# Kernel tuning notes

Hardware: AMD Instinct MI355X
Metric: run time of the kernel (lower is better)

The kernel has to match this reference:

```python
import jax, jax.numpy as jnp
import numpy as np
import math

N = 8192
IN_FEATURES = 512
OUT_FEATURES = 64
NEG_INF = -9e15

def setup_inputs() -> dict:
    key = jax.random.key(0)
    k1, k2, k3, k4 = jax.random.split(key, 4)
    inp = jax.random.normal(k1, (N, IN_FEATURES), dtype=jnp.float32)
    adj = jax.random.randint(k2, (N, N), 0, 2, dtype=jnp.int32)
    # xavier_uniform with gain=1.414 for [in, out] weights
    limit = 1.414 * math.sqrt(6.0 / (IN_FEATURES + OUT_FEATURES))
    kW = jax.random.uniform(k3, (IN_FEATURES, OUT_FEATURES), dtype=jnp.float32, minval=-limit, maxval=limit)
    vW = jax.random.uniform(k4, (IN_FEATURES, OUT_FEATURES), dtype=jnp.float32, minval=-limit, maxval=limit)
    return {"input": inp, "adj": adj, "kW": kW, "vW": vW}

def reference(input, adj, kW, vW):
    kh = input @ kW                      # [N, d]
    vh = input @ vW                      # [N, d]
    d = kh.shape[1]
    K = (kh @ kh.T) / jnp.sqrt(jnp.asarray(d, dtype=kh.dtype))  # [N, N]
    scores = jnp.where(adj > 0, K, jnp.asarray(NEG_INF, dtype=K.dtype))
    attention = jax.nn.softmax(scores, axis=1)
    # dropout is a no-op (p=0.0 / eval mode)
    h_prime = attention @ vh             # [N, d]
    return jax.nn.elu(h_prime)           # concat=True path
```

## Files before the change

kernel.cpp:

```cpp
#include <hip/hip_runtime.h>
#include <math.h>

typedef __bf16 bf16_t;
typedef __bf16 bf16x8 __attribute__((ext_vector_type(8)));
typedef float f32x4 __attribute__((ext_vector_type(4)));

#define NN 8192
#define L2E 1.44269504088896340736f
#define SMAX 45.0f
#define KSCALE 0.35355339059327373f

__global__ __launch_bounds__(256) void conv_kernel(
    const float* __restrict__ input,
    const float* __restrict__ kW,
    const float* __restrict__ vW,
    bf16_t* __restrict__ inputH,
    bf16_t* __restrict__ inputL,
    bf16_t* __restrict__ wimgH,
    bf16_t* __restrict__ wimgL)
{
    const int b = blockIdx.x;
    if (b < 2048) {
        const size_t idx = ((size_t)b * 256 + threadIdx.x) * 8;
        f32x4 a0 = *(const f32x4*)&input[idx];
        f32x4 a1 = *(const f32x4*)&input[idx + 4];
        bf16x8 h8, l8;
        #pragma unroll
        for (int j = 0; j < 4; ++j) {
            bf16_t h0 = (bf16_t)a0[j], h1 = (bf16_t)a1[j];
            h8[j]     = h0;  l8[j]     = (bf16_t)(a0[j] - (float)h0);
            h8[4 + j] = h1;  l8[4 + j] = (bf16_t)(a1[j] - (float)h1);
        }
        *(bf16x8*)&inputH[idx] = h8;
        *(bf16x8*)&inputL[idx] = l8;
    } else {
        const int gid  = (b - 2048) * 256 + threadIdx.x;
        const int proj = gid >> 12;
        const int r    = gid & 4095;
        const int frag = r >> 6;
        const int lane = r & 63;
        const int kc   = frag >> 2;
        const int nb   = frag & 3;
        const int quad = lane >> 4;
        const int l15  = lane & 15;
        const float* W = proj ? vW : kW;
        bf16x8 h8, l8;
        #pragma unroll
        for (int j = 0; j < 8; ++j) {
            float w  = W[(size_t)(kc * 32 + quad * 8 + j) * 64 + nb * 16 + l15];
            bf16_t h = (bf16_t)w;
            h8[j] = h;
            l8[j] = (bf16_t)(w - (float)h);
        }
        ((bf16x8*)wimgH)[gid] = h8;
        ((bf16x8*)wimgL)[gid] = l8;
    }
}

__global__ __launch_bounds__(256) void pack_adj(
    const int* __restrict__ adj, unsigned int* __restrict__ bits)
{
    const int lane = threadIdx.x & 63;
    const int gw   = blockIdx.x * 4 + (threadIdx.x >> 6);
    const int nw   = gridDim.x * 4;
    const int nchunks = (NN / 256) * NN;
    for (int c = gw; c < nchunks; c += nw) {
        const int* p = adj + (size_t)c * 256;
        unsigned int* o = bits + (size_t)c * 8;
        #pragma unroll
        for (int k = 0; k < 4; ++k) {
            int v = p[k * 64 + lane];
            unsigned long long m = __ballot(v > 0);
            if (lane == 0) *(uint2*)(o + 2 * k) = *(uint2*)&m;
        }
    }
}

__global__ __launch_bounds__(512) void proj_kernel(
    const bf16_t* __restrict__ inputH,
    const bf16_t* __restrict__ inputL,
    const bf16_t* __restrict__ wimgH,
    const bf16_t* __restrict__ wimgL,
    bf16_t* __restrict__ khs_hi,
    bf16_t* __restrict__ khs_lo,
    bf16_t* __restrict__ vhT)
{
    const int tid   = threadIdx.x;
    const int w     = tid >> 6;
    const int lane  = tid & 63;
    const int proj  = w >> 2;
    const int nb    = w & 3;
    const int l15   = lane & 15;
    const int quad  = lane >> 4;
    const int rbase = blockIdx.x * 16;

    const bf16x8* ah_p = (const bf16x8*)&inputH[(size_t)(rbase + l15) * 512 + quad * 8];
    const bf16x8* al_p = (const bf16x8*)&inputL[(size_t)(rbase + l15) * 512 + quad * 8];
    const bf16x8* bh_p = (const bf16x8*)wimgH + ((size_t)proj * 64 + nb) * 64 + lane;
    const bf16x8* bl_p = (const bf16x8*)wimgL + ((size_t)proj * 64 + nb) * 64 + lane;

    f32x4 acc = {};
    #pragma unroll
    for (int kc = 0; kc < 16; ++kc) {
        bf16x8 ah = ah_p[kc * 4];
        bf16x8 al = al_p[kc * 4];
        bf16x8 bh = bh_p[(size_t)kc * 256];
        bf16x8 bl = bl_p[(size_t)kc * 256];
        acc = __builtin_amdgcn_mfma_f32_16x16x32_bf16(ah, bh, acc, 0, 0, 0);
        acc = __builtin_amdgcn_mfma_f32_16x16x32_bf16(al, bh, acc, 0, 0, 0);
        acc = __builtin_amdgcn_mfma_f32_16x16x32_bf16(ah, bl, acc, 0, 0, 0);
    }

    const int dcol = nb * 16 + l15;
    if (proj == 0) {
        #pragma unroll
        for (int r = 0; r < 4; ++r) {
            float v  = acc[r] * KSCALE;
            bf16_t h = (bf16_t)v;
            khs_hi[(size_t)(rbase + quad * 4 + r) * 64 + dcol] = h;
            khs_lo[(size_t)(rbase + quad * 4 + r) * 64 + dcol] = (bf16_t)(v - (float)h);
        }
    } else {
        union { bf16_t b[4]; uint2 u; } pk;
        #pragma unroll
        for (int r = 0; r < 4; ++r) pk.b[r] = (bf16_t)acc[r];
        *(uint2*)&vhT[(size_t)dcol * NN + rbase + quad * 4] = pk.u;
    }
}

__global__ __launch_bounds__(512, 4) void attn_kernel(
    const unsigned int* __restrict__ bits,
    const bf16_t* __restrict__ khs_hi,
    const bf16_t* __restrict__ khs_lo,
    const bf16_t* __restrict__ vhT,
    float* __restrict__ out)
{
    __shared__ __align__(16) float PlBuf[8 * 1152];

    const int tid   = threadIdx.x;
    const int w     = tid >> 6;
    const int lane  = tid & 63;
    const int l15   = lane & 15;
    const int quad  = lane >> 4;
    const int qbase = blockIdx.x * 16;
    const int colstart = w * 1024;

    const bf16x8 qh0 = *(const bf16x8*)&khs_hi[(size_t)(qbase + l15) * 64 + quad * 8];
    const bf16x8 qh1 = *(const bf16x8*)&khs_hi[(size_t)(qbase + l15) * 64 + 32 + quad * 8];
    const bf16x8 ql0 = *(const bf16x8*)&khs_lo[(size_t)(qbase + l15) * 64 + quad * 8];
    const bf16x8 ql1 = *(const bf16x8*)&khs_lo[(size_t)(qbase + l15) * 64 + 32 + quad * 8];

    bf16x8 ones;
    #pragma unroll
    for (int j = 0; j < 8; ++j) ones[j] = (bf16_t)1.0f;

    f32x4 o0 = {}, o1 = {}, o2 = {}, o3 = {}, o4 = {};

    const unsigned int* bp = bits + (size_t)(qbase + quad * 4) * 256 + (colstart >> 5);

    unsigned int wcur[4], wnxt[4];
    #pragma unroll
    for (int r = 0; r < 4; ++r) wcur[r] = bp[r * 256];

    for (int t = 0; t < 32; ++t) {
        const int colbase = colstart + t * 32;
        float* Plw = &PlBuf[w * 1152 + (t & 1) * 576];

        const bf16_t* kph = khs_hi + (size_t)(colbase + l15) * 64 + quad * 8;
        bf16x8 bh00 = *(const bf16x8*)(kph);
        bf16x8 bh01 = *(const bf16x8*)(kph + 32);
        bf16x8 bh10 = *(const bf16x8*)(kph + 16 * 64);
        bf16x8 bh11 = *(const bf16x8*)(kph + 16 * 64 + 32);
        const bf16_t* vp = vhT + (size_t)l15 * NN + colbase + quad * 8;
        bf16x8 bv0 = *(const bf16x8*)(vp);
        bf16x8 bv1 = *(const bf16x8*)(vp + (size_t)16 * NN);
        bf16x8 bv2 = *(const bf16x8*)(vp + (size_t)32 * NN);
        bf16x8 bv3 = *(const bf16x8*)(vp + (size_t)48 * NN);

        const int tn = (t + 1) & 31;
        #pragma unroll
        for (int r = 0; r < 4; ++r) wnxt[r] = bp[r * 256 + tn];

        f32x4 zz = {};
        f32x4 s0 = __builtin_amdgcn_mfma_f32_16x16x32_bf16(qh0, bh00, zz, 0, 0, 0);
        s0 = __builtin_amdgcn_mfma_f32_16x16x32_bf16(qh1, bh01, s0, 0, 0, 0);
        s0 = __builtin_amdgcn_mfma_f32_16x16x32_bf16(ql0, bh00, s0, 0, 0, 0);
        s0 = __builtin_amdgcn_mfma_f32_16x16x32_bf16(ql1, bh01, s0, 0, 0, 0);
        f32x4 s1 = __builtin_amdgcn_mfma_f32_16x16x32_bf16(qh0, bh10, zz, 0, 0, 0);
        s1 = __builtin_amdgcn_mfma_f32_16x16x32_bf16(qh1, bh11, s1, 0, 0, 0);
        s1 = __builtin_amdgcn_mfma_f32_16x16x32_bf16(ql0, bh10, s1, 0, 0, 0);
        s1 = __builtin_amdgcn_mfma_f32_16x16x32_bf16(ql1, bh11, s1, 0, 0, 0);

        #pragma unroll
        for (int r = 0; r < 4; ++r) {
            float p0 = ((wcur[r] >> l15) & 1u)        ? __builtin_amdgcn_exp2f((s0[r] - SMAX) * L2E) : 0.f;
            float p1 = ((wcur[r] >> (16 + l15)) & 1u) ? __builtin_amdgcn_exp2f((s1[r] - SMAX) * L2E) : 0.f;
            Plw[(quad * 4 + r) * 36 + l15]      = p0;
            Plw[(quad * 4 + r) * 36 + 16 + l15] = p1;
        }

        __asm__ __volatile__("s_waitcnt lgkmcnt(0)" ::: "memory");

        f32x4 pfa = *(const f32x4*)&Plw[l15 * 36 + quad * 8];
        f32x4 pfb = *(const f32x4*)&Plw[l15 * 36 + quad * 8 + 4];
        bf16x8 pa;
        #pragma unroll
        for (int j = 0; j < 4; ++j) { pa[j] = (bf16_t)pfa[j]; pa[4 + j] = (bf16_t)pfb[j]; }

        o0 = __builtin_amdgcn_mfma_f32_16x16x32_bf16(pa, bv0, o0, 0, 0, 0);
        o1 = __builtin_amdgcn_mfma_f32_16x16x32_bf16(pa, bv1, o1, 0, 0, 0);
        o2 = __builtin_amdgcn_mfma_f32_16x16x32_bf16(pa, bv2, o2, 0, 0, 0);
        o3 = __builtin_amdgcn_mfma_f32_16x16x32_bf16(pa, bv3, o3, 0, 0, 0);
        o4 = __builtin_amdgcn_mfma_f32_16x16x32_bf16(pa, ones, o4, 0, 0, 0);

        #pragma unroll
        for (int r = 0; r < 4; ++r) wcur[r] = wnxt[r];
    }

    float* M = PlBuf;
    #pragma unroll
    for (int s = 4; s >= 1; s >>= 1) {
        __syncthreads();
        if (w >= s && w < 2 * s) {
            float* base = M + (w - s) * 16 * 68;
            #pragma unroll
            for (int r = 0; r < 4; ++r) {
                const int row = quad * 4 + r;
                base[row * 68 + l15]      = o0[r];
                base[row * 68 + 16 + l15] = o1[r];
                base[row * 68 + 32 + l15] = o2[r];
                base[row * 68 + 48 + l15] = o3[r];
                if (l15 == 0) base[row * 68 + 64] = o4[r];
            }
        }
        __syncthreads();
        if (w < s) {
            float* base = M + w * 16 * 68;
            #pragma unroll
            for (int r = 0; r < 4; ++r) {
                const int row = quad * 4 + r;
                o0[r] += base[row * 68 + l15];
                o1[r] += base[row * 68 + 16 + l15];
                o2[r] += base[row * 68 + 32 + l15];
                o3[r] += base[row * 68 + 48 + l15];
                o4[r] += base[row * 68 + 64];
            }
        }
    }

    if (w == 0) {
        #pragma unroll
        for (int r = 0; r < 4; ++r) {
            const size_t row = (size_t)qbase + quad * 4 + r;
            float l   = o4[r];
            float inv = 1.0f / (l > 0.f ? l : 1.0f);
            float v0 = o0[r] * inv, v1 = o1[r] * inv, v2 = o2[r] * inv, v3 = o3[r] * inv;
            out[row * 64 + l15]      = v0 > 0.f ? v0 : expm1f(v0);
            out[row * 64 + 16 + l15] = v1 > 0.f ? v1 : expm1f(v1);
            out[row * 64 + 32 + l15] = v2 > 0.f ? v2 : expm1f(v2);
            out[row * 64 + 48 + l15] = v3 > 0.f ? v3 : expm1f(v3);
        }
    }
}

extern "C" void kernel_launch(void* const* d_in, const int* in_sizes, int n_in,
                              void* d_out, int out_size, void* d_ws, size_t ws_size,
                              hipStream_t stream) {
    const float* input = nullptr;
    const int*   adj   = nullptr;
    const float* kW    = nullptr;
    const float* vW    = nullptr;
    for (int i = 0; i < n_in; ++i) {
        if (in_sizes[i] == 8192 * 512)            input = (const float*)d_in[i];
        else if (in_sizes[i] == 512 * 64) {
            if (!kW) kW = (const float*)d_in[i]; else vW = (const float*)d_in[i];
        } else                                    adj = (const int*)d_in[i];
    }
    float* out = (float*)d_out;

    char* ws = (char*)d_ws;
    bf16_t*       khs_hi = (bf16_t*)(ws);
    bf16_t*       khs_lo = (bf16_t*)(ws + (1u << 20));
    bf16_t*       vhT    = (bf16_t*)(ws + (2u << 20));
    unsigned int* bits   = (unsigned int*)(ws + (3u << 20));
    bf16_t*       inputH = (bf16_t*)(ws + (11u << 20));
    bf16_t*       inputL = (bf16_t*)(ws + (19u << 20));
    bf16_t*       wimgH  = (bf16_t*)(ws + (27u << 20));
    bf16_t*       wimgL  = (bf16_t*)(ws + (27u << 20) + (128u << 10));

    conv_kernel<<<2080, 256, 0, stream>>>(input, kW, vW, inputH, inputL, wimgH, wimgL);
    pack_adj<<<2048, 256, 0, stream>>>(adj, bits);
    proj_kernel<<<512, 512, 0, stream>>>(inputH, inputL, wimgH, wimgL, khs_hi, khs_lo, vhT);
    attn_kernel<<<512, 512, 0, stream>>>(bits, khs_hi, khs_lo, vhT, out);
}
```

Before: 529.7 us.

## Split attention columns across two blocks with atomic accumulation and fuse prep kernels

The attention kernel now gives each 16-row block two column halves handled by separate blocks, doubling the grid and halving the loop length. Partial numerators and denominators are combined with atomicAdd into a zeroed workspace, and a new finalize kernel applies normalization and ELU. The input/weight conversion, adjacency bit-packing and accumulator zeroing are merged into one launch to cut launch overhead. The aim is better CU utilization for the attention stage, at the cost of atomic traffic, an extra finalize kernel and a tighter occupancy hint.

```diff
diff --git a/kernel.cpp b/kernel.cpp
--- a/kernel.cpp
+++ b/kernel.cpp
@@ -9,15 +9,19 @@
 #define L2E 1.44269504088896340736f
 #define SMAX 45.0f
 #define KSCALE 0.35355339059327373f
-
-__global__ __launch_bounds__(256) void conv_kernel(
+#define ACCW 66
+
+__global__ __launch_bounds__(256) void prep_kernel(
     const float* __restrict__ input,
     const float* __restrict__ kW,
     const float* __restrict__ vW,
+    const int*   __restrict__ adj,
     bf16_t* __restrict__ inputH,
     bf16_t* __restrict__ inputL,
     bf16_t* __restrict__ wimgH,
-    bf16_t* __restrict__ wimgL)
+    bf16_t* __restrict__ wimgL,
+    unsigned int* __restrict__ bits,
+    float* __restrict__ acc)
 {
     const int b = blockIdx.x;
     if (b < 2048) {
@@ -33,7 +37,7 @@
         }
         *(bf16x8*)&inputH[idx] = h8;
         *(bf16x8*)&inputL[idx] = l8;
-    } else {
+    } else if (b < 2080) {
         const int gid  = (b - 2048) * 256 + threadIdx.x;
         const int proj = gid >> 12;
         const int r    = gid & 4095;
@@ -54,25 +58,25 @@
         }
         ((bf16x8*)wimgH)[gid] = h8;
         ((bf16x8*)wimgL)[gid] = l8;
-    }
-}
-
-__global__ __launch_bounds__(256) void pack_adj(
-    const int* __restrict__ adj, unsigned int* __restrict__ bits)
-{
-    const int lane = threadIdx.x & 63;
-    const int gw   = blockIdx.x * 4 + (threadIdx.x >> 6);
-    const int nw   = gridDim.x * 4;
-    const int nchunks = (NN / 256) * NN;
-    for (int c = gw; c < nchunks; c += nw) {
-        const int* p = adj + (size_t)c * 256;
-        unsigned int* o = bits + (size_t)c * 8;
-        #pragma unroll
-        for (int k = 0; k < 4; ++k) {
-            int v = p[k * 64 + lane];
-            unsigned long long m = __ballot(v > 0);
-            if (lane == 0) *(uint2*)(o + 2 * k) = *(uint2*)&m;
-        }
+    } else if (b < 4128) {
+        const int lane = threadIdx.x & 63;
+        const int gw   = (b - 2080) * 4 + (threadIdx.x >> 6);
+        const int nw   = 2048 * 4;
+        const int nchunks = (NN / 256) * NN;
+        for (int c = gw; c < nchunks; c += nw) {
+            const int* p = adj + (size_t)c * 256;
+            unsigned int* o = bits + (size_t)c * 8;
+            #pragma unroll
+            for (int k = 0; k < 4; ++k) {
+                int v = p[k * 64 + lane];
+                unsigned long long m = __ballot(v > 0);
+                if (lane == 0) *(uint2*)(o + 2 * k) = *(uint2*)&m;
+            }
+        }
+    } else {
+        const size_t idx = ((size_t)(b - 4128) * 256 + threadIdx.x) * 4;
+        f32x4 z = {};
+        *(f32x4*)&acc[idx] = z;
     }
 }
 
@@ -128,12 +132,12 @@
     }
 }
 
-__global__ __launch_bounds__(512, 4) void attn_kernel(
+__global__ __launch_bounds__(512, 8) void attn_kernel(
     const unsigned int* __restrict__ bits,
     const bf16_t* __restrict__ khs_hi,
     const bf16_t* __restrict__ khs_lo,
     const bf16_t* __restrict__ vhT,
-    float* __restrict__ out)
+    float* __restrict__ acc)
 {
     __shared__ __align__(16) float PlBuf[8 * 1152];
 
@@ -142,8 +146,10 @@
     const int lane  = tid & 63;
     const int l15   = lane & 15;
     const int quad  = lane >> 4;
-    const int qbase = blockIdx.x * 16;
-    const int colstart = w * 1024;
+    const int rb    = blockIdx.x >> 1;
+    const int ch    = blockIdx.x & 1;
+    const int qbase = rb * 16;
+    const int colstart = ch * 4096 + w * 512;
 
     const bf16x8 qh0 = *(const bf16x8*)&khs_hi[(size_t)(qbase + l15) * 64 + quad * 8];
     const bf16x8 qh1 = *(const bf16x8*)&khs_hi[(size_t)(qbase + l15) * 64 + 32 + quad * 8];
@@ -162,7 +168,7 @@
     #pragma unroll
     for (int r = 0; r < 4; ++r) wcur[r] = bp[r * 256];
 
-    for (int t = 0; t < 32; ++t) {
+    for (int t = 0; t < 16; ++t) {
         const int colbase = colstart + t * 32;
         float* Plw = &PlBuf[w * 1152 + (t & 1) * 576];
 
@@ -177,7 +183,7 @@
         bf16x8 bv2 = *(const bf16x8*)(vp + (size_t)32 * NN);
         bf16x8 bv3 = *(const bf16x8*)(vp + (size_t)48 * NN);
 
-        const int tn = (t + 1) & 31;
+        const int tn = (t + 1) & 15;
         #pragma unroll
         for (int r = 0; r < 4; ++r) wnxt[r] = bp[r * 256 + tn];
 
@@ -252,15 +258,21 @@
         #pragma unroll
         for (int r = 0; r < 4; ++r) {
             const size_t row = (size_t)qbase + quad * 4 + r;
-            float l   = o4[r];
-            float inv = 1.0f / (l > 0.f ? l : 1.0f);
-            float v0 = o0[r] * inv, v1 = o1[r] * inv, v2 = o2[r] * inv, v3 = o3[r] * inv;
-            out[row * 64 + l15]      = v0 > 0.f ? v0 : expm1f(v0);
-            out[row * 64 + 16 + l15] = v1 > 0.f ? v1 : expm1f(v1);
-            out[row * 64 + 32 + l15] = v2 > 0.f ? v2 : expm1f(v2);
-            out[row * 64 + 48 + l15] = v3 > 0.f ? v3 : expm1f(v3);
-        }
-    }
+            atomicAdd(&acc[row * ACCW + l15],      o0[r]);
+            atomicAdd(&acc[row * ACCW + 16 + l15], o1[r]);
+            atomicAdd(&acc[row * ACCW + 32 + l15], o2[r]);
+            atomicAdd(&acc[row * ACCW + 48 + l15], o3[r]);
+            if (l15 == 0) atomicAdd(&acc[row * ACCW + 64], o4[r]);
+        }
+    }
+}
+
+__global__ void finalize(const float* __restrict__ acc, float* __restrict__ out) {
+    int i = blockIdx.x * blockDim.x + threadIdx.x;
+    int row = i >> 6, d = i & 63;
+    float l = acc[(size_t)row * ACCW + 64];
+    float v = acc[(size_t)row * ACCW + d] / (l > 0.f ? l : 1.f);
+    out[i] = v > 0.f ? v : expm1f(v);
 }
 
 extern "C" void kernel_launch(void* const* d_in, const int* in_sizes, int n_in,
@@ -287,9 +299,11 @@
     bf16_t*       inputL = (bf16_t*)(ws + (19u << 20));
     bf16_t*       wimgH  = (bf16_t*)(ws + (27u << 20));
     bf16_t*       wimgL  = (bf16_t*)(ws + (27u << 20) + (128u << 10));
-
-    conv_kernel<<<2080, 256, 0, stream>>>(input, kW, vW, inputH, inputL, wimgH, wimgL);
-    pack_adj<<<2048, 256, 0, stream>>>(adj, bits);
+    float*        acc    = (float*)(ws + (28u << 20));
+
+    prep_kernel<<<4656, 256, 0, stream>>>(input, kW, vW, adj,
+                                          inputH, inputL, wimgH, wimgL, bits, acc);
     proj_kernel<<<512, 512, 0, stream>>>(inputH, inputL, wimgH, wimgL, khs_hi, khs_lo, vhT);
-    attn_kernel<<<512, 512, 0, stream>>>(bits, khs_hi, khs_lo, vhT, out);
-}
+    attn_kernel<<<1024, 512, 0, stream>>>(bits, khs_hi, khs_lo, vhT, acc);
+    finalize<<<(NN * 64) / 512, 512, 0, stream>>>(acc, out);
+}
```

Result: slower. 623.7 us (+17.7%).

## Fuse adjacency packing into prep kernel and swap LDS P round-trip for bpermute

Applied to the files above, without the earlier changes.

The adjacency bit-packing kernel is merged into the input/weight conversion kernel as extra blocks, which removes one launch and lets the two independent prep jobs run concurrently. In the attention kernel the score MFMA operands are swapped so each lane holds a transposed score tile. The probabilities are packed to bf16 in registers and redistributed with ds_bpermute instead of being written to LDS as floats and read back. This cuts LDS traffic and the explicit waitcnt, and shrinks shared memory, which may allow more occupancy. The cost is eight bpermutes per step and some select logic.

```diff
diff --git a/kernel.cpp b/kernel.cpp
--- a/kernel.cpp
+++ b/kernel.cpp
@@ -10,14 +10,16 @@
 #define SMAX 45.0f
 #define KSCALE 0.35355339059327373f
 
-__global__ __launch_bounds__(256) void conv_kernel(
+__global__ __launch_bounds__(256) void prep_kernel(
     const float* __restrict__ input,
     const float* __restrict__ kW,
     const float* __restrict__ vW,
+    const int*   __restrict__ adj,
     bf16_t* __restrict__ inputH,
     bf16_t* __restrict__ inputL,
     bf16_t* __restrict__ wimgH,
-    bf16_t* __restrict__ wimgL)
+    bf16_t* __restrict__ wimgL,
+    unsigned int* __restrict__ bits)
 {
     const int b = blockIdx.x;
     if (b < 2048) {
@@ -33,7 +35,7 @@
         }
         *(bf16x8*)&inputH[idx] = h8;
         *(bf16x8*)&inputL[idx] = l8;
-    } else {
+    } else if (b < 2080) {
         const int gid  = (b - 2048) * 256 + threadIdx.x;
         const int proj = gid >> 12;
         const int r    = gid & 4095;
@@ -54,24 +56,20 @@
         }
         ((bf16x8*)wimgH)[gid] = h8;
         ((bf16x8*)wimgL)[gid] = l8;
-    }
-}
-
-__global__ __launch_bounds__(256) void pack_adj(
-    const int* __restrict__ adj, unsigned int* __restrict__ bits)
-{
-    const int lane = threadIdx.x & 63;
-    const int gw   = blockIdx.x * 4 + (threadIdx.x >> 6);
-    const int nw   = gridDim.x * 4;
-    const int nchunks = (NN / 256) * NN;
-    for (int c = gw; c < nchunks; c += nw) {
-        const int* p = adj + (size_t)c * 256;
-        unsigned int* o = bits + (size_t)c * 8;
-        #pragma unroll
-        for (int k = 0; k < 4; ++k) {
-            int v = p[k * 64 + lane];
-            unsigned long long m = __ballot(v > 0);
-            if (lane == 0) *(uint2*)(o + 2 * k) = *(uint2*)&m;
+    } else {
+        const int lane = threadIdx.x & 63;
+        const int gw   = (b - 2080) * 4 + (threadIdx.x >> 6);
+        const int nw   = 2048 * 4;
+        const int nchunks = (NN / 256) * NN;
+        for (int c = gw; c < nchunks; c += nw) {
+            const int* p = adj + (size_t)c * 256;
+            unsigned int* o = bits + (size_t)c * 8;
+            #pragma unroll
+            for (int k = 0; k < 4; ++k) {
+                int v = p[k * 64 + lane];
+                unsigned long long m = __ballot(v > 0);
+                if (lane == 0) *(uint2*)(o + 2 * k) = *(uint2*)&m;
+            }
         }
     }
 }
@@ -135,7 +133,7 @@
     const bf16_t* __restrict__ vhT,
     float* __restrict__ out)
 {
-    __shared__ __align__(16) float PlBuf[8 * 1152];
+    __shared__ __align__(16) float M[4 * 16 * 68];
 
     const int tid   = threadIdx.x;
     const int w     = tid >> 6;
@@ -156,15 +154,14 @@
 
     f32x4 o0 = {}, o1 = {}, o2 = {}, o3 = {}, o4 = {};
 
-    const unsigned int* bp = bits + (size_t)(qbase + quad * 4) * 256 + (colstart >> 5);
-
-    unsigned int wcur[4], wnxt[4];
-    #pragma unroll
-    for (int r = 0; r < 4; ++r) wcur[r] = bp[r * 256];
+    const unsigned int* bpl = bits + (size_t)(qbase + l15) * 256 + (colstart >> 5);
+    unsigned int mcur = bpl[0], mnxt;
+
+    const int idxA = (l15 + (((2 * quad)    ) & 3) * 16) * 4;
+    const int idxB = (l15 + (((2 * quad) | 1) & 3) * 16) * 4;
 
     for (int t = 0; t < 32; ++t) {
         const int colbase = colstart + t * 32;
-        float* Plw = &PlBuf[w * 1152 + (t & 1) * 576];
 
         const bf16_t* kph = khs_hi + (size_t)(colbase + l15) * 64 + quad * 8;
         bf16x8 bh00 = *(const bf16x8*)(kph);
@@ -177,47 +174,53 @@
         bf16x8 bv2 = *(const bf16x8*)(vp + (size_t)32 * NN);
         bf16x8 bv3 = *(const bf16x8*)(vp + (size_t)48 * NN);
 
-        const int tn = (t + 1) & 31;
-        #pragma unroll
-        for (int r = 0; r < 4; ++r) wnxt[r] = bp[r * 256 + tn];
+        mnxt = bpl[(t + 1) & 31];
 
         f32x4 zz = {};
-        f32x4 s0 = __builtin_amdgcn_mfma_f32_16x16x32_bf16(qh0, bh00, zz, 0, 0, 0);
-        s0 = __builtin_amdgcn_mfma_f32_16x16x32_bf16(qh1, bh01, s0, 0, 0, 0);
-        s0 = __builtin_amdgcn_mfma_f32_16x16x32_bf16(ql0, bh00, s0, 0, 0, 0);
-        s0 = __builtin_amdgcn_mfma_f32_16x16x32_bf16(ql1, bh01, s0, 0, 0, 0);
-        f32x4 s1 = __builtin_amdgcn_mfma_f32_16x16x32_bf16(qh0, bh10, zz, 0, 0, 0);
-        s1 = __builtin_amdgcn_mfma_f32_16x16x32_bf16(qh1, bh11, s1, 0, 0, 0);
-        s1 = __builtin_amdgcn_mfma_f32_16x16x32_bf16(ql0, bh10, s1, 0, 0, 0);
-        s1 = __builtin_amdgcn_mfma_f32_16x16x32_bf16(ql1, bh11, s1, 0, 0, 0);
-
+        f32x4 s0 = __builtin_amdgcn_mfma_f32_16x16x32_bf16(bh00, qh0, zz, 0, 0, 0);
+        s0 = __builtin_amdgcn_mfma_f32_16x16x32_bf16(bh01, qh1, s0, 0, 0, 0);
+        s0 = __builtin_amdgcn_mfma_f32_16x16x32_bf16(bh00, ql0, s0, 0, 0, 0);
+        s0 = __builtin_amdgcn_mfma_f32_16x16x32_bf16(bh01, ql1, s0, 0, 0, 0);
+        f32x4 s1 = __builtin_amdgcn_mfma_f32_16x16x32_bf16(bh10, qh0, zz, 0, 0, 0);
+        s1 = __builtin_amdgcn_mfma_f32_16x16x32_bf16(bh11, qh1, s1, 0, 0, 0);
+        s1 = __builtin_amdgcn_mfma_f32_16x16x32_bf16(bh10, ql0, s1, 0, 0, 0);
+        s1 = __builtin_amdgcn_mfma_f32_16x16x32_bf16(bh11, ql1, s1, 0, 0, 0);
+
+        union { bf16_t b[2]; int u; } k0, k1, k2, k3;
         #pragma unroll
         for (int r = 0; r < 4; ++r) {
-            float p0 = ((wcur[r] >> l15) & 1u)        ? __builtin_amdgcn_exp2f((s0[r] - SMAX) * L2E) : 0.f;
-            float p1 = ((wcur[r] >> (16 + l15)) & 1u) ? __builtin_amdgcn_exp2f((s1[r] - SMAX) * L2E) : 0.f;
-            Plw[(quad * 4 + r) * 36 + l15]      = p0;
-            Plw[(quad * 4 + r) * 36 + 16 + l15] = p1;
-        }
-
-        __asm__ __volatile__("s_waitcnt lgkmcnt(0)" ::: "memory");
-
-        f32x4 pfa = *(const f32x4*)&Plw[l15 * 36 + quad * 8];
-        f32x4 pfb = *(const f32x4*)&Plw[l15 * 36 + quad * 8 + 4];
-        bf16x8 pa;
-        #pragma unroll
-        for (int j = 0; j < 4; ++j) { pa[j] = (bf16_t)pfa[j]; pa[4 + j] = (bf16_t)pfb[j]; }
-
-        o0 = __builtin_amdgcn_mfma_f32_16x16x32_bf16(pa, bv0, o0, 0, 0, 0);
-        o1 = __builtin_amdgcn_mfma_f32_16x16x32_bf16(pa, bv1, o1, 0, 0, 0);
-        o2 = __builtin_amdgcn_mfma_f32_16x16x32_bf16(pa, bv2, o2, 0, 0, 0);
-        o3 = __builtin_amdgcn_mfma_f32_16x16x32_bf16(pa, bv3, o3, 0, 0, 0);
-        o4 = __builtin_amdgcn_mfma_f32_16x16x32_bf16(pa, ones, o4, 0, 0, 0);
-
-        #pragma unroll
-        for (int r = 0; r < 4; ++r) wcur[r] = wnxt[r];
-    }
-
-    float* M = PlBuf;
+            float p0 = ((mcur >> (quad * 4 + r)) & 1u)
+                         ? __builtin_amdgcn_exp2f((s0[r] - SMAX) * L2E) : 0.f;
+            float p1 = ((mcur >> (16 + quad * 4 + r)) & 1u)
+                         ? __builtin_amdgcn_exp2f((s1[r] - SMAX) * L2E) : 0.f;
+            if (r < 2) { k0.b[r] = (bf16_t)p0; k2.b[r] = (bf16_t)p1; }
+            else       { k1.b[r - 2] = (bf16_t)p0; k3.b[r - 2] = (bf16_t)p1; }
+        }
+
+        int a0 = __builtin_amdgcn_ds_bpermute(idxA, k0.u);
+        int a1 = __builtin_amdgcn_ds_bpermute(idxA, k1.u);
+        int a2 = __builtin_amdgcn_ds_bpermute(idxB, k0.u);
+        int a3 = __builtin_amdgcn_ds_bpermute(idxB, k1.u);
+        int c0 = __builtin_amdgcn_ds_bpermute(idxA, k2.u);
+        int c1 = __builtin_amdgcn_ds_bpermute(idxA, k3.u);
+        int c2 = __builtin_amdgcn_ds_bpermute(idxB, k2.u);
+        int c3 = __builtin_amdgcn_ds_bpermute(idxB, k3.u);
+
+        union { int u[4]; bf16x8 v; } pa;
+        pa.u[0] = quad < 2 ? a0 : c0;
+        pa.u[1] = quad < 2 ? a1 : c1;
+        pa.u[2] = quad < 2 ? a2 : c2;
+        pa.u[3] = quad < 2 ? a3 : c3;
+
+        o0 = __builtin_amdgcn_mfma_f32_16x16x32_bf16(pa.v, bv0, o0, 0, 0, 0);
+        o1 = __builtin_amdgcn_mfma_f32_16x16x32_bf16(pa.v, bv1, o1, 0, 0, 0);
+        o2 = __builtin_amdgcn_mfma_f32_16x16x32_bf16(pa.v, bv2, o2, 0, 0, 0);
+        o3 = __builtin_amdgcn_mfma_f32_16x16x32_bf16(pa.v, bv3, o3, 0, 0, 0);
+        o4 = __builtin_amdgcn_mfma_f32_16x16x32_bf16(pa.v, ones, o4, 0, 0, 0);
+
+        mcur = mnxt;
+    }
+
     #pragma unroll
     for (int s = 4; s >= 1; s >>= 1) {
         __syncthreads();
@@ -288,8 +291,8 @@
     bf16_t*       wimgH  = (bf16_t*)(ws + (27u << 20));
     bf16_t*       wimgL  = (bf16_t*)(ws + (27u << 20) + (128u << 10));
 
-    conv_kernel<<<2080, 256, 0, stream>>>(input, kW, vW, inputH, inputL, wimgH, wimgL);
-    pack_adj<<<2048, 256, 0, stream>>>(adj, bits);
+    prep_kernel<<<4128, 256, 0, stream>>>(input, kW, vW, adj,
+                                          inputH, inputL, wimgH, wimgL, bits);
     proj_kernel<<<512, 512, 0, stream>>>(inputH, inputL, wimgH, wimgL, khs_hi, khs_lo, vhT);
     attn_kernel<<<512, 512, 0, stream>>>(bits, khs_hi, khs_lo, vhT, out);
 }
```

After: 537.2 us. No clear change (+1.4%).
